# Performance work log

Measured on AMD Instinct MI355X. Metric: run time of the kernel, lower is better.

## Reference

```python
import jax, jax.numpy as jnp
import numpy as np

E = 128  # embed_size


def setup_inputs() -> dict:
    key = jax.random.key(0)
    ks = jax.random.split(key, 20)
    NU, NI, NEV = 100000, 50000, 4096
    s = 0.05  # weight scale so softplus(dot) stays well-conditioned
    inp = {
        "user_emb": jax.random.normal(ks[0], (NU, E), jnp.float32) * s,
        "item_emb": jax.random.normal(ks[1], (NI, E), jnp.float32) * s,
        "ugru_wi": jax.random.normal(ks[2], (3 * E, E), jnp.float32) * s,
        "ugru_wh": jax.random.normal(ks[3], (3 * E, E), jnp.float32) * s,
        "ugru_bi": jax.random.normal(ks[4], (3 * E,), jnp.float32) * s,
        "ugru_bh": jax.random.normal(ks[5], (3 * E,), jnp.float32) * s,
        "igru_wi": jax.random.normal(ks[6], (3 * E, E), jnp.float32) * s,
        "igru_wh": jax.random.normal(ks[7], (3 * E, E), jnp.float32) * s,
        "igru_bi": jax.random.normal(ks[8], (3 * E,), jnp.float32) * s,
        "igru_bh": jax.random.normal(ks[9], (3 * E,), jnp.float32) * s,
        "t1_w": jax.random.normal(ks[10], (E, 2 * E), jnp.float32) * s,
        "t1_b": jax.random.normal(ks[11], (E,), jnp.float32) * s,
        "t2_w": jax.random.normal(ks[12], (32, E), jnp.float32) * s,
        "t2_b": jax.random.normal(ks[13], (32,), jnp.float32) * s,
        "t3_w": jax.random.normal(ks[14], (1, 32), jnp.float32) * s,
        "t3_b": jax.random.normal(ks[15], (1,), jnp.float32) * s,
        "user_ids": jax.random.randint(ks[16], (NEV,), 0, NU, jnp.int32),
        "item_ids": jax.random.randint(ks[17], (NEV,), 0, NI, jnp.int32),
    }
    return inp


def _gru(x, h, wi, wh, bi, bh):
    # torch.nn.GRUCell math, single sample: x,h [E]; wi,wh [3E,E]
    gi = wi @ x + bi
    gh = wh @ h + bh
    ir, iz, inn = jnp.split(gi, 3)
    hr, hz, hn = jnp.split(gh, 3)
    r = jax.nn.sigmoid(ir + hr)
    z = jax.nn.sigmoid(iz + hz)
    n = jnp.tanh(inn + r * hn)
    return (1.0 - z) * n + z * h


def reference(user_emb, item_emb, ugru_wi, ugru_wh, ugru_bi, ugru_bh,
              igru_wi, igru_wh, igru_bi, igru_bh,
              t1_w, t1_b, t2_w, t2_b, t3_w, t3_b,
              user_ids, item_ids):
    # Sequential event processing: per-event gather of user/item embedding,
    # Rayleigh base compatibility score, MLP (transForm1/2/3) branch score,
    # coupled GRUCell updates scattered back into the embedding tables.
    def step(carry, ev):
        U, V = carry
        u_id, i_id = ev
        u = U[u_id]          # [E] gather (dict-cache lookup in original)
        v = V[i_id]          # [E]
        comp = jax.nn.softplus(jnp.dot(u, v)) + 1e-10  # base_compatibility
        loss = -jnp.log(comp)                           # -log p(event)
        cat = jnp.concatenate([u, v])                   # [2E]
        h = jax.nn.relu(t1_w @ cat + t1_b)              # transForm1 + act
        h = jax.nn.relu(t2_w @ h + t2_b)                # transForm2 + act
        score = jax.nn.sigmoid(t3_w @ h + t3_b)[0]      # transForm3
        nu = _gru(v, u, ugru_wi, ugru_wh, ugru_bi, ugru_bh)  # user_cell
        nv = _gru(u, v, igru_wi, igru_wh, igru_bi, igru_bh)  # item_cell
        U = U.at[u_id].set(nu)  # coevolution scatter
        V = V.at[i_id].set(nv)
        return (U, V), jnp.stack([loss, score])

    (_, _), outs = jax.lax.scan(step, (user_emb, item_emb),
                                (user_ids, item_ids))
    return outs  # [num_events, 2] : (-log comp, branch score)
```

## Files before the change

kernel.cpp:

```cpp
#include <hip/hip_runtime.h>
#include <math.h>

#define EMB 128
#define MAXEV 4096
#define GEV 16

struct Hdr { int nl0; int nl1; int ncomp2; };

typedef __attribute__((ext_vector_type(8))) short bf16x8;
typedef __attribute__((ext_vector_type(4))) float f32x4;

__device__ __forceinline__ float sigmoidf_(float x) { return 1.0f / (1.0f + expf(-x)); }
__device__ __forceinline__ float softplusf_(float x) {
    return (x > 0.f) ? x + log1pf(expf(-x)) : log1pf(expf(x));
}
__device__ __forceinline__ unsigned short f2bf(float f) {
    unsigned int u = __float_as_uint(f);
    u += 0x7FFFu + ((u >> 16) & 1u);
    return (unsigned short)(u >> 16);
}
__device__ __forceinline__ float bf2f(unsigned short s) {
    return __uint_as_float((unsigned int)s << 16);
}

__global__ __launch_bounds__(64) void prev_kernel(
    const int* __restrict__ uids, const int* __restrict__ iids,
    int* __restrict__ prevu, int* __restrict__ previ, int nev,
    const float* __restrict__ Wuh, const float* __restrict__ Wii,
    const float* __restrict__ Wui, const float* __restrict__ Wih,
    const float* __restrict__ T1w, const float* __restrict__ T2w,
    unsigned short* __restrict__ wb_uh, unsigned short* __restrict__ wb_ii,
    unsigned short* __restrict__ wb_ui, unsigned short* __restrict__ wb_ih,
    unsigned short* __restrict__ t1wb, unsigned short* __restrict__ t2wb)
{
    int t = blockIdx.x;
    int lane = threadIdx.x;

    {
        int gid = t * 64 + lane;
        if (gid < 58368) {
            const float* src; unsigned short* dst; int q;
            if (gid < 49152) {
                int m = gid / 12288; q = gid - m * 12288;
                src = (m == 0) ? Wuh : (m == 1) ? Wii : (m == 2) ? Wui : Wih;
                dst = (m == 0) ? wb_uh : (m == 1) ? wb_ii : (m == 2) ? wb_ui : wb_ih;
            } else if (gid < 57344) { q = gid - 49152; src = T1w; dst = t1wb; }
            else                    { q = gid - 57344; src = T2w; dst = t2wb; }
            float4 v = ((const float4*)src)[q];
            *(ushort4*)(dst + (size_t)q * 4) =
                make_ushort4(f2bf(v.x), f2bf(v.y), f2bf(v.z), f2bf(v.w));
        }
    }

    if (t >= nev) return;
    int myu = uids[t], myi = iids[t];
    int bu = -1, bi = -1;
    for (int j = lane; j < t; j += 64) {
        if (uids[j] == myu) bu = j;
        if (iids[j] == myi) bi = j;
    }
    for (int off = 32; off; off >>= 1) {
        bu = max(bu, __shfl_xor(bu, off));
        bi = max(bi, __shfl_xor(bi, off));
    }
    if (lane == 0) { prevu[t] = bu; previ[t] = bi; }
}

__global__ __launch_bounds__(1024) void setup_kernel(
    const int* __restrict__ prevu, const int* __restrict__ previ,
    int* __restrict__ order0, int* __restrict__ order1,
    int* __restrict__ tail2Order, int* __restrict__ compStart,
    Hdr* __restrict__ hdr, int nev)
{
    __shared__ int   lab[MAXEV];
    __shared__ int   tmpT[MAXEV];
    __shared__ int   t2l[MAXEV];
    __shared__ short slev[MAXEV];
    __shared__ int   schanged, sn0, sn1, sn2, sntl;

    int tid = threadIdx.x;
    for (int t = tid; t < nev; t += 1024) slev[t] = 0;
    if (tid == 0) { sn0 = 0; sn1 = 0; sn2 = 0; sntl = 0; }
    __syncthreads();

    for (int t = tid; t < nev; t += 1024) {
        if (prevu[t] >= 0 || previ[t] >= 0) tmpT[atomicAdd(&sntl, 1)] = t;
        else                                 order0[atomicAdd(&sn0, 1)] = t;
    }
    __syncthreads();
    int ntl = sntl;

    for (int it = 0; it < nev; ++it) {
        if (tid == 0) schanged = 0;
        __syncthreads();
        for (int i = tid; i < ntl; i += 1024) {
            int t = tmpT[i];
            int pu = prevu[t], pi = previ[t];
            int nl = 0;
            if (pu >= 0) nl = slev[pu] + 1;
            if (pi >= 0) { int c = slev[pi] + 1; nl = nl > c ? nl : c; }
            if (nl > (int)slev[t]) { slev[t] = (short)nl; schanged = 1; }
        }
        __syncthreads();
        if (!schanged) break;
        __syncthreads();
    }

    for (int i = tid; i < ntl; i += 1024) {
        int t = tmpT[i];
        if (slev[t] == 1)      order1[atomicAdd(&sn1, 1)] = t;
        else if (slev[t] >= 2) t2l[atomicAdd(&sn2, 1)] = t;
    }
    __syncthreads();
    int n2 = sn2;

    for (int i = tid; i < n2; i += 1024) lab[t2l[i]] = t2l[i];
    __syncthreads();
    for (int it = 0; it < nev; ++it) {
        if (tid == 0) schanged = 0;
        __syncthreads();
        for (int i = tid; i < n2; i += 1024) {
            int t = t2l[i];
            int m = lab[t];
            int pu = prevu[t], pi = previ[t];
            bool eu = (pu >= 0 && slev[pu] >= 2);
            bool ei = (pi >= 0 && slev[pi] >= 2);
            if (eu) m = min(m, lab[pu]);
            if (ei) m = min(m, lab[pi]);
            if (m < lab[t]) { atomicMin(&lab[t], m); schanged = 1; }
            if (eu && m < lab[pu]) { atomicMin(&lab[pu], m); schanged = 1; }
            if (ei && m < lab[pi]) { atomicMin(&lab[pi], m); schanged = 1; }
        }
        __syncthreads();
        if (!schanged) break;
        __syncthreads();
    }

    for (int i = tid; i < n2; i += 1024) tmpT[i] = (lab[t2l[i]] << 12) | t2l[i];
    __syncthreads();
    for (int i = tid; i < n2; i += 1024) {
        int k = tmpT[i], r = 0;
        for (int j = 0; j < n2; ++j) r += (tmpT[j] < k);
        tail2Order[r] = k & 0xFFF;
    }
    __syncthreads();

    if (tid == 0) {
        int nc = 0;
        for (int i = 0; i < n2; ++i)
            if (i == 0 || lab[tail2Order[i]] != lab[tail2Order[i - 1]])
                compStart[nc++] = i;
        compStart[nc] = n2;
        hdr->ncomp2 = nc;
        hdr->nl0 = sn0;
        hdr->nl1 = sn1;
    }
}

__global__ __launch_bounds__(256) void gru_fused_kernel(
    const float* __restrict__ U0, const float* __restrict__ V0,
    const unsigned short* __restrict__ wb_ui, const unsigned short* __restrict__ wb_uh,
    const unsigned short* __restrict__ wb_ii, const unsigned short* __restrict__ wb_ih,
    const float* __restrict__ bui, const float* __restrict__ buh,
    const float* __restrict__ bii, const float* __restrict__ bih,
    const unsigned short* __restrict__ t1wb, const float* __restrict__ T1b,
    const unsigned short* __restrict__ t2wb, const float* __restrict__ T2b,
    const float* __restrict__ T3w, const float* __restrict__ T3b,
    const int* __restrict__ uids, const int* __restrict__ iids,
    const int* __restrict__ prevu, const int* __restrict__ previ,
    const float* NUr, const float* NVr,
    const int* __restrict__ order, const int* __restrict__ cnt_p,
    float* NU, float* NV, float* __restrict__ out)
{
    __shared__ __align__(16) unsigned short xbu[GEV][136];
    __shared__ __align__(16) unsigned short xbv[GEV][136];
    __shared__ __align__(16) float gg[GEV][772];
    unsigned short (*h1b)[136] = (unsigned short (*)[136])&gg[0][0];
    float (*h2s)[36] = (float (*)[36])&gg[2][0];

    int cnt = *cnt_p;
    int e0 = blockIdx.x * GEV;
    if (e0 >= cnt) return;

    int tid = threadIdx.x;
    int ev = tid >> 4, c8 = (tid & 15) * 8;

    {
        int e = e0 + ev;
        int t = -1;
        float4 a0, a1, c0, c1;
        if (e < cnt) {
            t = order[e];
            int pu = prevu[t], pi = previ[t];
            const float* up = (pu < 0 ? U0 + (size_t)uids[t] * EMB : NUr + (size_t)pu * EMB) + c8;
            const float* vp = (pi < 0 ? V0 + (size_t)iids[t] * EMB : NVr + (size_t)pi * EMB) + c8;
            a0 = ((const float4*)up)[0]; a1 = ((const float4*)up)[1];
            c0 = ((const float4*)vp)[0]; c1 = ((const float4*)vp)[1];
        } else {
            a0 = make_float4(0.f, 0.f, 0.f, 0.f); a1 = a0; c0 = a0; c1 = a0;
        }
        *(ushort4*)&xbu[ev][c8]     = make_ushort4(f2bf(a0.x), f2bf(a0.y), f2bf(a0.z), f2bf(a0.w));
        *(ushort4*)&xbu[ev][c8 + 4] = make_ushort4(f2bf(a1.x), f2bf(a1.y), f2bf(a1.z), f2bf(a1.w));
        *(ushort4*)&xbv[ev][c8]     = make_ushort4(f2bf(c0.x), f2bf(c0.y), f2bf(c0.z), f2bf(c0.w));
        *(ushort4*)&xbv[ev][c8 + 4] = make_ushort4(f2bf(c1.x), f2bf(c1.y), f2bf(c1.z), f2bf(c1.w));
        float dp = a0.x * c0.x + a0.y * c0.y + a0.z * c0.z + a0.w * c0.w
                 + a1.x * c1.x + a1.y * c1.y + a1.z * c1.z + a1.w * c1.w;
        dp += __shfl_xor(dp, 1); dp += __shfl_xor(dp, 2);
        dp += __shfl_xor(dp, 4); dp += __shfl_xor(dp, 8);
        if ((tid & 15) == 0 && t >= 0)
            out[2 * (size_t)t] = -logf(softplusf_(dp) + 1e-10f);
    }
    __syncthreads();

    int w = tid >> 6, l = tid & 63;
    int lr = l & 15, lk = (l >> 4) * 8;

    for (int ph = 0; ph < 2; ++ph) {
        const unsigned short* Wi = ph ? wb_ii : wb_ui;
        const unsigned short* Wh = ph ? wb_ih : wb_uh;
        const unsigned short (*Xi)[136] = ph ? xbu : xbv;
        const unsigned short (*Xh)[136] = ph ? xbv : xbu;

        f32x4 acc[12] = {};
        #pragma unroll
        for (int kk = 0; kk < 4; ++kk) {
            bf16x8 ai = *(const bf16x8*)&Xi[lr][kk * 32 + lk];
            bf16x8 ah = *(const bf16x8*)&Xh[lr][kk * 32 + lk];
            #pragma unroll
            for (int j = 0; j < 12; ++j) {
                int nt = w * 12 + j;
                bool ish = nt >= 24;
                int brow = (ish ? nt - 24 : nt) * 16 + lr;
                const unsigned short* W = ish ? Wh : Wi;
                bf16x8 b = *(const bf16x8*)(W + (size_t)brow * EMB + kk * 32 + lk);
                acc[j] = __builtin_amdgcn_mfma_f32_16x16x32_bf16(ish ? ah : ai, b, acc[j], 0, 0, 0);
            }
        }
        #pragma unroll
        for (int j = 0; j < 12; ++j) {
            int nt = w * 12 + j;
            #pragma unroll
            for (int i = 0; i < 4; ++i)
                gg[(l >> 4) * 4 + i][nt * 16 + lr] = acc[j][i];
        }
        __syncthreads();

        {
            int e = e0 + ev;
            if (e < cnt) {
                int t = order[e];
                const float* bi = ph ? bii : bui;
                const float* bh = ph ? bih : buh;
                float* N = ph ? NV : NU;
                const unsigned short (*xh)[136] = ph ? xbv : xbu;
                #pragma unroll
                for (int i = 0; i < 8; ++i) {
                    int ch = c8 + i;
                    float r_ = sigmoidf_(gg[ev][ch] + bi[ch] + gg[ev][384 + ch] + bh[ch]);
                    float z_ = sigmoidf_(gg[ev][128 + ch] + bi[128 + ch] + gg[ev][512 + ch] + bh[128 + ch]);
                    float n_ = tanhf(gg[ev][256 + ch] + bi[256 + ch] + r_ * (gg[ev][640 + ch] + bh[256 + ch]));
                    float h = bf2f(xh[ev][ch]);
                    N[(size_t)t * EMB + ch] = (1.f - z_) * n_ + z_ * h;
                }
            }
        }
        __syncthreads();
    }

    {
        f32x4 acc1[2] = {};
        #pragma unroll
        for (int kh = 0; kh < 8; ++kh) {
            bf16x8 a = (kh < 4) ? *(const bf16x8*)&xbu[lr][kh * 32 + lk]
                                : *(const bf16x8*)&xbv[lr][(kh - 4) * 32 + lk];
            #pragma unroll
            for (int n = 0; n < 2; ++n) {
                int nt = w * 2 + n;
                bf16x8 b = *(const bf16x8*)(t1wb + (size_t)(nt * 16 + lr) * 256 + kh * 32 + lk);
                acc1[n] = __builtin_amdgcn_mfma_f32_16x16x32_bf16(a, b, acc1[n], 0, 0, 0);
            }
        }
        #pragma unroll
        for (int n = 0; n < 2; ++n) {
            int col = (w * 2 + n) * 16 + lr;
            float bb = T1b[col];
            #pragma unroll
            for (int i = 0; i < 4; ++i)
                h1b[(l >> 4) * 4 + i][col] = f2bf(fmaxf(acc1[n][i] + bb, 0.f));
        }
    }
    __syncthreads();

    if (w < 2) {
        f32x4 acc2 = {};
        #pragma unroll
        for (int kk = 0; kk < 4; ++kk) {
            bf16x8 a = *(const bf16x8*)&h1b[lr][kk * 32 + lk];
            bf16x8 b = *(const bf16x8*)(t2wb + (size_t)(w * 16 + lr) * 128 + kk * 32 + lk);
            acc2 = __builtin_amdgcn_mfma_f32_16x16x32_bf16(a, b, acc2, 0, 0, 0);
        }
        int col = w * 16 + lr;
        float bb = T2b[col];
        #pragma unroll
        for (int i = 0; i < 4; ++i)
            h2s[(l >> 4) * 4 + i][col] = fmaxf(acc2[i] + bb, 0.f);
    }
    __syncthreads();

    if (tid < 64) {
        int evl = tid >> 2, q4 = tid & 3;
        float p = 0.f;
        #pragma unroll
        for (int i = 0; i < 8; ++i) {
            int ch = q4 * 8 + i;
            p = fmaf(T3w[ch], h2s[evl][ch], p);
        }
        p += __shfl_xor(p, 1); p += __shfl_xor(p, 2);
        int e = e0 + evl;
        if (q4 == 0 && e < cnt)
            out[2 * (size_t)order[e] + 1] = sigmoidf_(p + T3b[0]);
    }
}

__global__ __launch_bounds__(1024) void tail2_kernel(
    const float* __restrict__ U0,  const float* __restrict__ V0,
    const unsigned short* __restrict__ wb_ui, const unsigned short* __restrict__ wb_uh,
    const float* __restrict__ bui, const float* __restrict__ buh,
    const unsigned short* __restrict__ wb_ii, const unsigned short* __restrict__ wb_ih,
    const float* __restrict__ bii, const float* __restrict__ bih,
    const unsigned short* __restrict__ t1wb, const float* __restrict__ T1b,
    const float* __restrict__ T2w, const float* __restrict__ T2b,
    const float* __restrict__ T3w, const float* __restrict__ T3b,
    const int* __restrict__ uids,  const int* __restrict__ iids,
    const int* __restrict__ prevu, const int* __restrict__ previ,
    const int* __restrict__ tail2Order, const int* __restrict__ compStart,
    const Hdr* __restrict__ hdr,
    float* __restrict__ NU, float* __restrict__ NV, float* __restrict__ out)
{
    __shared__ __align__(16) float su[EMB];
    __shared__ __align__(16) float sv[EMB];
    __shared__ float gg[1536];
    int tid = threadIdx.x;
    int ncomp = hdr->ncomp2;

    int g = tid >> 4, j = tid & 15;
    int mat = g >> 4;
    const unsigned short* W = (mat == 0) ? wb_ui : (mat == 1) ? wb_uh
                            : (mat == 2) ? wb_ii : wb_ih;

    for (int c = blockIdx.x; c < ncomp; c += gridDim.x) {
        int kb = compStart[c], ke = compStart[c + 1];
        for (int k = kb; k < ke; ++k) {
            int t = tail2Order[k];
            int pu = prevu[t], pi = previ[t];
            const float* up = (pu < 0) ? U0 + (size_t)uids[t] * EMB : NU + (size_t)pu * EMB;
            const float* vp = (pi < 0) ? V0 + (size_t)iids[t] * EMB : NV + (size_t)pi * EMB;
            __syncthreads();
            if (tid < EMB)        su[tid] = up[tid];
            else if (tid < 2*EMB) sv[tid - EMB] = vp[tid - EMB];
            __syncthreads();

            const float* x = (mat == 1 || mat == 2) ? su : sv;
            float x8[8];
            #pragma unroll
            for (int i = 0; i < 8; ++i) x8[i] = x[j * 8 + i];

            #pragma unroll 1
            for (int b = 0; b < 2; ++b) {
                int rbase = (g & 15) * 24 + b * 12;
                bf16x8 wv[12];
                #pragma unroll
                for (int q = 0; q < 12; ++q)
                    wv[q] = *(const bf16x8*)(W + (size_t)(rbase + q) * EMB + j * 8);
                #pragma unroll
                for (int q = 0; q < 12; ++q) {
                    float s = bf2f((unsigned short)wv[q][0]) * x8[0]
                            + bf2f((unsigned short)wv[q][1]) * x8[1]
                            + bf2f((unsigned short)wv[q][2]) * x8[2]
                            + bf2f((unsigned short)wv[q][3]) * x8[3]
                            + bf2f((unsigned short)wv[q][4]) * x8[4]
                            + bf2f((unsigned short)wv[q][5]) * x8[5]
                            + bf2f((unsigned short)wv[q][6]) * x8[6]
                            + bf2f((unsigned short)wv[q][7]) * x8[7];
                    s += __shfl_xor(s, 1); s += __shfl_xor(s, 2);
                    s += __shfl_xor(s, 4); s += __shfl_xor(s, 8);
                    if (j == (q & 15)) gg[mat * 384 + rbase + q] = s;
                }
            }
            __syncthreads();

            if (tid < EMB) {
                int e = tid;
                float r_ = sigmoidf_(gg[e] + bui[e] + gg[384 + e] + buh[e]);
                float z_ = sigmoidf_(gg[128 + e] + bui[128 + e] + gg[512 + e] + buh[128 + e]);
                float n_ = tanhf(gg[256 + e] + bui[256 + e] + r_ * (gg[640 + e] + buh[256 + e]));
                NU[(size_t)t * EMB + e] = (1.f - z_) * n_ + z_ * su[e];
            } else if (tid < 2*EMB) {
                int e = tid - EMB;
                float r_ = sigmoidf_(gg[768 + e] + bii[e] + gg[1152 + e] + bih[e]);
                float z_ = sigmoidf_(gg[896 + e] + bii[128 + e] + gg[1280 + e] + bih[128 + e]);
                float n_ = tanhf(gg[1024 + e] + bii[256 + e] + r_ * (gg[1408 + e] + bih[256 + e]));
                NV[(size_t)t * EMB + e] = (1.f - z_) * n_ + z_ * sv[e];
            }
            __syncthreads();

            if (tid < 64) {
                float p = su[tid] * sv[tid] + su[tid + 64] * sv[tid + 64];
                p += __shfl_xor(p, 1);  p += __shfl_xor(p, 2);
                p += __shfl_xor(p, 4);  p += __shfl_xor(p, 8);
                p += __shfl_xor(p, 16); p += __shfl_xor(p, 32);
                if (tid == 0) out[2 * (size_t)t] = -logf(softplusf_(p) + 1e-10f);
            }
            {
                int r = tid >> 3, kq = tid & 7;
                const float* xx = (kq < 4) ? su : sv;
                int off = (kq < 4) ? 0 : 128;
                float s = 0.f;
                #pragma unroll
                for (int m = 0; m < 4; ++m) {
                    bf16x8 wv = *(const bf16x8*)(t1wb + (size_t)r * 256 + kq * 32 + m * 8);
                    #pragma unroll
                    for (int i = 0; i < 8; ++i)
                        s = fmaf(bf2f((unsigned short)wv[i]),
                                 xx[kq * 32 + m * 8 + i - off], s);
                }
                s += __shfl_xor(s, 1); s += __shfl_xor(s, 2); s += __shfl_xor(s, 4);
                if (kq == 0) gg[r] = fmaxf(s + T1b[r], 0.f);
            }
            __syncthreads();
            {
                int r2 = tid >> 5, kq = tid & 31;
                float4 wv = *(const float4*)(T2w + (size_t)r2 * 128 + kq * 4);
                float s = wv.x * gg[kq * 4]     + wv.y * gg[kq * 4 + 1]
                        + wv.z * gg[kq * 4 + 2] + wv.w * gg[kq * 4 + 3];
                s += __shfl_xor(s, 1); s += __shfl_xor(s, 2);
                s += __shfl_xor(s, 4); s += __shfl_xor(s, 8); s += __shfl_xor(s, 16);
                if (kq == 0) gg[200 + r2] = fmaxf(s + T2b[r2], 0.f);
            }
            __syncthreads();
            if (tid < 32) {
                float p = T3w[tid] * gg[200 + tid];
                p += __shfl_xor(p, 1); p += __shfl_xor(p, 2);
                p += __shfl_xor(p, 4); p += __shfl_xor(p, 8); p += __shfl_xor(p, 16);
                if (tid == 0) out[2 * (size_t)t + 1] = sigmoidf_(p + T3b[0]);
            }
        }
    }
}

extern "C" void kernel_launch(void* const* d_in, const int* in_sizes, int n_in,
                              void* d_out, int out_size, void* d_ws, size_t ws_size,
                              hipStream_t stream)
{
    const float* U0  = (const float*)d_in[0];
    const float* V0  = (const float*)d_in[1];
    const float* Wui = (const float*)d_in[2];
    const float* Wuh = (const float*)d_in[3];
    const float* bui = (const float*)d_in[4];
    const float* buh = (const float*)d_in[5];
    const float* Wii = (const float*)d_in[6];
    const float* Wih = (const float*)d_in[7];
    const float* bii = (const float*)d_in[8];
    const float* bih = (const float*)d_in[9];
    const float* T1w = (const float*)d_in[10];
    const float* T1b = (const float*)d_in[11];
    const float* T2w = (const float*)d_in[12];
    const float* T2b = (const float*)d_in[13];
    const float* T3w = (const float*)d_in[14];
    const float* T3b = (const float*)d_in[15];
    const int* uids  = (const int*)d_in[16];
    const int* iids  = (const int*)d_in[17];
    int nev = in_sizes[16];

    char* ws = (char*)d_ws;
    int* base = (int*)ws;
    int* prevu      = base;
    int* previ      = base + MAXEV;
    int* order0     = base + 2 * MAXEV;
    int* order1     = base + 3 * MAXEV;
    int* tail2Order = base + 4 * MAXEV;
    int* compStart  = base + 5 * MAXEV;
    Hdr* hdr        = (Hdr*)(base + 6 * MAXEV + 4);
    float* NU = (float*)(ws + (160 << 10));
    float* NV = NU + (size_t)MAXEV * EMB;
    unsigned short* wb_uh = (unsigned short*)(NV + (size_t)MAXEV * EMB);
    unsigned short* wb_ii = wb_uh + 384 * EMB;
    unsigned short* wb_ui = wb_ii + 384 * EMB;
    unsigned short* wb_ih = wb_ui + 384 * EMB;
    unsigned short* t1wb  = wb_ih + 384 * EMB;
    unsigned short* t2wb  = t1wb + EMB * 256;
    float* out = (float*)d_out;

    prev_kernel<<<MAXEV, 64, 0, stream>>>(
        uids, iids, prevu, previ, nev,
        Wuh, Wii, Wui, Wih, T1w, T2w,
        wb_uh, wb_ii, wb_ui, wb_ih, t1wb, t2wb);
    setup_kernel<<<1, 1024, 0, stream>>>(prevu, previ, order0, order1,
                                         tail2Order, compStart, hdr, nev);

    gru_fused_kernel<<<MAXEV / GEV, 256, 0, stream>>>(
        U0, V0, wb_ui, wb_uh, wb_ii, wb_ih, bui, buh, bii, bih,
        t1wb, T1b, t2wb, T2b, T3w, T3b,
        uids, iids, prevu, previ, NU, NV, order0, &hdr->nl0, NU, NV, out);

    gru_fused_kernel<<<MAXEV / GEV, 256, 0, stream>>>(
        U0, V0, wb_ui, wb_uh, wb_ii, wb_ih, bui, buh, bii, bih,
        t1wb, T1b, t2wb, T2b, T3w, T3b,
        uids, iids, prevu, previ, NU, NV, order1, &hdr->nl1, NU, NV, out);

    tail2_kernel<<<64, 1024, 0, stream>>>(
        U0, V0, wb_ui, wb_uh, bui, buh, wb_ii, wb_ih, bii, bih,
        t1wb, T1b, T2w, T2b, T3w, T3b,
        uids, iids, prevu, previ, tail2Order, compStart, hdr, NU, NV, out);
}
```

Baseline: 101.7 us.

## Move MLP and loss out of serial tail GRU loop into batched per-wave pass

The tail kernel now runs only the GRU updates in its serial per-component loop. Afterward it computes the base loss and the three-layer MLP score for 16 events at a time, one wavefront per event, by regathering the pre-update embeddings into shared memory. This shortens the serial dependency chain and removes several block-wide barriers from each step. The second MLP layer now uses bf16 weights instead of fp32, which adds small rounding differences.

```diff
diff --git a/kernel.cpp b/kernel.cpp
--- a/kernel.cpp
+++ b/kernel.cpp
@@ -329,7 +329,7 @@
     const unsigned short* __restrict__ wb_ii, const unsigned short* __restrict__ wb_ih,
     const float* __restrict__ bii, const float* __restrict__ bih,
     const unsigned short* __restrict__ t1wb, const float* __restrict__ T1b,
-    const float* __restrict__ T2w, const float* __restrict__ T2b,
+    const unsigned short* __restrict__ t2wb, const float* __restrict__ T2b,
     const float* __restrict__ T3w, const float* __restrict__ T3b,
     const int* __restrict__ uids,  const int* __restrict__ iids,
     const int* __restrict__ prevu, const int* __restrict__ previ,
@@ -340,6 +340,8 @@
     __shared__ __align__(16) float su[EMB];
     __shared__ __align__(16) float sv[EMB];
     __shared__ float gg[1536];
+    __shared__ __align__(16) float sxe[16][256];
+    __shared__ float sh1[16][EMB];
     int tid = threadIdx.x;
     int ncomp = hdr->ncomp2;
 
@@ -350,6 +352,7 @@
 
     for (int c = blockIdx.x; c < ncomp; c += gridDim.x) {
         int kb = compStart[c], ke = compStart[c + 1];
+
         for (int k = kb; k < ke; ++k) {
             int t = tail2Order[k];
             int pu = prevu[t], pi = previ[t];
@@ -402,47 +405,67 @@
                 float n_ = tanhf(gg[1024 + e] + bii[256 + e] + r_ * (gg[1408 + e] + bih[256 + e]));
                 NV[(size_t)t * EMB + e] = (1.f - z_) * n_ + z_ * sv[e];
             }
-            __syncthreads();
-
-            if (tid < 64) {
-                float p = su[tid] * sv[tid] + su[tid + 64] * sv[tid + 64];
-                p += __shfl_xor(p, 1);  p += __shfl_xor(p, 2);
-                p += __shfl_xor(p, 4);  p += __shfl_xor(p, 8);
-                p += __shfl_xor(p, 16); p += __shfl_xor(p, 32);
-                if (tid == 0) out[2 * (size_t)t] = -logf(softplusf_(p) + 1e-10f);
-            }
-            {
-                int r = tid >> 3, kq = tid & 7;
-                const float* xx = (kq < 4) ? su : sv;
-                int off = (kq < 4) ? 0 : 128;
-                float s = 0.f;
-                #pragma unroll
-                for (int m = 0; m < 4; ++m) {
-                    bf16x8 wv = *(const bf16x8*)(t1wb + (size_t)r * 256 + kq * 32 + m * 8);
-                    #pragma unroll
-                    for (int i = 0; i < 8; ++i)
-                        s = fmaf(bf2f((unsigned short)wv[i]),
-                                 xx[kq * 32 + m * 8 + i - off], s);
-                }
-                s += __shfl_xor(s, 1); s += __shfl_xor(s, 2); s += __shfl_xor(s, 4);
-                if (kq == 0) gg[r] = fmaxf(s + T1b[r], 0.f);
-            }
+        }
+
+        for (int kk0 = kb; kk0 < ke; kk0 += 16) {
             __syncthreads();
             {
-                int r2 = tid >> 5, kq = tid & 31;
-                float4 wv = *(const float4*)(T2w + (size_t)r2 * 128 + kq * 4);
-                float s = wv.x * gg[kq * 4]     + wv.y * gg[kq * 4 + 1]
-                        + wv.z * gg[kq * 4 + 2] + wv.w * gg[kq * 4 + 3];
-                s += __shfl_xor(s, 1); s += __shfl_xor(s, 2);
-                s += __shfl_xor(s, 4); s += __shfl_xor(s, 8); s += __shfl_xor(s, 16);
-                if (kq == 0) gg[200 + r2] = fmaxf(s + T2b[r2], 0.f);
+                int ev = tid >> 6, c4 = (tid & 63) * 4;
+                int k = kk0 + ev;
+                if (k < ke) {
+                    int t = tail2Order[k];
+                    int pu = prevu[t], pi = previ[t];
+                    const float* up = (pu < 0) ? U0 + (size_t)uids[t] * EMB : NU + (size_t)pu * EMB;
+                    const float* vp = (pi < 0) ? V0 + (size_t)iids[t] * EMB : NV + (size_t)pi * EMB;
+                    const float* src = (c4 < EMB) ? up + c4 : vp + (c4 - EMB);
+                    *(float4*)&sxe[ev][c4] = *(const float4*)src;
+                }
             }
             __syncthreads();
-            if (tid < 32) {
-                float p = T3w[tid] * gg[200 + tid];
-                p += __shfl_xor(p, 1); p += __shfl_xor(p, 2);
-                p += __shfl_xor(p, 4); p += __shfl_xor(p, 8); p += __shfl_xor(p, 16);
-                if (tid == 0) out[2 * (size_t)t + 1] = sigmoidf_(p + T3b[0]);
+
+            int wv2 = tid >> 6, l = tid & 63;
+            int k = kk0 + wv2;
+            if (k < ke) {
+                int t = tail2Order[k];
+                const float* sx = sxe[wv2];
+                {
+                    float p = sx[l] * sx[128 + l] + sx[l + 64] * sx[192 + l];
+                    p += __shfl_xor(p, 1);  p += __shfl_xor(p, 2);
+                    p += __shfl_xor(p, 4);  p += __shfl_xor(p, 8);
+                    p += __shfl_xor(p, 16); p += __shfl_xor(p, 32);
+                    if (l == 0) out[2 * (size_t)t] = -logf(softplusf_(p) + 1e-10f);
+                }
+                {
+                    float s0 = 0.f, s1 = 0.f;
+                    #pragma unroll 4
+                    for (int m = 0; m < 32; ++m) {
+                        bf16x8 w0 = *(const bf16x8*)(t1wb + (size_t)l * 256 + m * 8);
+                        bf16x8 w1 = *(const bf16x8*)(t1wb + (size_t)(l + 64) * 256 + m * 8);
+                        #pragma unroll
+                        for (int i = 0; i < 8; ++i) {
+                            float xv = sx[m * 8 + i];
+                            s0 = fmaf(bf2f((unsigned short)w0[i]), xv, s0);
+                            s1 = fmaf(bf2f((unsigned short)w1[i]), xv, s1);
+                        }
+                    }
+                    sh1[wv2][l]      = fmaxf(s0 + T1b[l], 0.f);
+                    sh1[wv2][l + 64] = fmaxf(s1 + T1b[l + 64], 0.f);
+                }
+                if (l < 32) {
+                    float s = 0.f;
+                    #pragma unroll 4
+                    for (int m = 0; m < 16; ++m) {
+                        bf16x8 wv = *(const bf16x8*)(t2wb + (size_t)l * 128 + m * 8);
+                        #pragma unroll
+                        for (int i = 0; i < 8; ++i)
+                            s = fmaf(bf2f((unsigned short)wv[i]), sh1[wv2][m * 8 + i], s);
+                    }
+                    float h2 = fmaxf(s + T2b[l], 0.f);
+                    float p = T3w[l] * h2;
+                    p += __shfl_xor(p, 1); p += __shfl_xor(p, 2);
+                    p += __shfl_xor(p, 4); p += __shfl_xor(p, 8); p += __shfl_xor(p, 16);
+                    if (l == 0) out[2 * (size_t)t + 1] = sigmoidf_(p + T3b[0]);
+                }
             }
         }
     }
@@ -510,6 +533,6 @@
 
     tail2_kernel<<<64, 1024, 0, stream>>>(
         U0, V0, wb_ui, wb_uh, bui, buh, wb_ii, wb_ih, bii, bih,
-        t1wb, T1b, T2w, T2b, T3w, T3b,
+        t1wb, T1b, t2wb, T2b, T3w, T3b,
         uids, iids, prevu, previ, tail2Order, compStart, hdr, NU, NV, out);
 }
```

After: 104.2 us. 2.4% more time.

## Drop level-1 batch pass; route all dependent events through component tail kernel

Applied to the files above, without the earlier changes.

The level-based split is removed. Events with no prior occurrence go to the batched GRU kernel, and every dependent event is grouped into connected components that the sequential tail kernel processes. This drops one launch of the fused kernel and the level-propagation loop in setup, and the tail grid grows from 64 to 256 blocks to cover the larger set of components. The trade-off is that level-1 events, which used to be batched, now run one at a time inside their component, and the O(n^2) rank sort now runs over more elements.

```diff
diff --git a/kernel.cpp b/kernel.cpp
--- a/kernel.cpp
+++ b/kernel.cpp
@@ -5,7 +5,7 @@
 #define MAXEV 4096
 #define GEV 16
 
-struct Hdr { int nl0; int nl1; int ncomp2; };
+struct Hdr { int nl0; int ncomp; };
 
 typedef __attribute__((ext_vector_type(8))) short bf16x8;
 typedef __attribute__((ext_vector_type(4))) float f32x4;
@@ -68,63 +68,39 @@
 
 __global__ __launch_bounds__(1024) void setup_kernel(
     const int* __restrict__ prevu, const int* __restrict__ previ,
-    int* __restrict__ order0, int* __restrict__ order1,
-    int* __restrict__ tail2Order, int* __restrict__ compStart,
-    Hdr* __restrict__ hdr, int nev)
+    int* __restrict__ order0, int* __restrict__ tailOrder,
+    int* __restrict__ compStart, Hdr* __restrict__ hdr, int nev)
 {
-    __shared__ int   lab[MAXEV];
-    __shared__ int   tmpT[MAXEV];
-    __shared__ int   t2l[MAXEV];
-    __shared__ short slev[MAXEV];
-    __shared__ int   schanged, sn0, sn1, sn2, sntl;
+    __shared__ int  lab[MAXEV];
+    __shared__ int  tmpT[MAXEV];
+    __shared__ int  t2l[MAXEV];
+    __shared__ char istail[MAXEV];
+    __shared__ int  schanged, sn0, sntl;
 
     int tid = threadIdx.x;
-    for (int t = tid; t < nev; t += 1024) slev[t] = 0;
-    if (tid == 0) { sn0 = 0; sn1 = 0; sn2 = 0; sntl = 0; }
+    if (tid == 0) { sn0 = 0; sntl = 0; }
     __syncthreads();
 
     for (int t = tid; t < nev; t += 1024) {
-        if (prevu[t] >= 0 || previ[t] >= 0) tmpT[atomicAdd(&sntl, 1)] = t;
-        else                                 order0[atomicAdd(&sn0, 1)] = t;
+        bool tl = (prevu[t] >= 0 || previ[t] >= 0);
+        istail[t] = tl;
+        if (tl) t2l[atomicAdd(&sntl, 1)] = t;
+        else    order0[atomicAdd(&sn0, 1)] = t;
     }
     __syncthreads();
     int ntl = sntl;
 
+    for (int i = tid; i < ntl; i += 1024) lab[t2l[i]] = t2l[i];
+    __syncthreads();
     for (int it = 0; it < nev; ++it) {
         if (tid == 0) schanged = 0;
         __syncthreads();
         for (int i = tid; i < ntl; i += 1024) {
-            int t = tmpT[i];
-            int pu = prevu[t], pi = previ[t];
-            int nl = 0;
-            if (pu >= 0) nl = slev[pu] + 1;
-            if (pi >= 0) { int c = slev[pi] + 1; nl = nl > c ? nl : c; }
-            if (nl > (int)slev[t]) { slev[t] = (short)nl; schanged = 1; }
-        }
-        __syncthreads();
-        if (!schanged) break;
-        __syncthreads();
-    }
-
-    for (int i = tid; i < ntl; i += 1024) {
-        int t = tmpT[i];
-        if (slev[t] == 1)      order1[atomicAdd(&sn1, 1)] = t;
-        else if (slev[t] >= 2) t2l[atomicAdd(&sn2, 1)] = t;
-    }
-    __syncthreads();
-    int n2 = sn2;
-
-    for (int i = tid; i < n2; i += 1024) lab[t2l[i]] = t2l[i];
-    __syncthreads();
-    for (int it = 0; it < nev; ++it) {
-        if (tid == 0) schanged = 0;
-        __syncthreads();
-        for (int i = tid; i < n2; i += 1024) {
             int t = t2l[i];
             int m = lab[t];
             int pu = prevu[t], pi = previ[t];
-            bool eu = (pu >= 0 && slev[pu] >= 2);
-            bool ei = (pi >= 0 && slev[pi] >= 2);
+            bool eu = (pu >= 0 && istail[pu]);
+            bool ei = (pi >= 0 && istail[pi]);
             if (eu) m = min(m, lab[pu]);
             if (ei) m = min(m, lab[pi]);
             if (m < lab[t]) { atomicMin(&lab[t], m); schanged = 1; }
@@ -136,24 +112,23 @@
         __syncthreads();
     }
 
-    for (int i = tid; i < n2; i += 1024) tmpT[i] = (lab[t2l[i]] << 12) | t2l[i];
-    __syncthreads();
-    for (int i = tid; i < n2; i += 1024) {
+    for (int i = tid; i < ntl; i += 1024) tmpT[i] = (lab[t2l[i]] << 12) | t2l[i];
+    __syncthreads();
+    for (int i = tid; i < ntl; i += 1024) {
         int k = tmpT[i], r = 0;
-        for (int j = 0; j < n2; ++j) r += (tmpT[j] < k);
-        tail2Order[r] = k & 0xFFF;
+        for (int j = 0; j < ntl; ++j) r += (tmpT[j] < k);
+        tailOrder[r] = k & 0xFFF;
     }
     __syncthreads();
 
     if (tid == 0) {
         int nc = 0;
-        for (int i = 0; i < n2; ++i)
-            if (i == 0 || lab[tail2Order[i]] != lab[tail2Order[i - 1]])
+        for (int i = 0; i < ntl; ++i)
+            if (i == 0 || lab[tailOrder[i]] != lab[tailOrder[i - 1]])
                 compStart[nc++] = i;
-        compStart[nc] = n2;
-        hdr->ncomp2 = nc;
+        compStart[nc] = ntl;
+        hdr->ncomp = nc;
         hdr->nl0 = sn0;
-        hdr->nl1 = sn1;
     }
 }
 
@@ -167,10 +142,8 @@
     const unsigned short* __restrict__ t2wb, const float* __restrict__ T2b,
     const float* __restrict__ T3w, const float* __restrict__ T3b,
     const int* __restrict__ uids, const int* __restrict__ iids,
-    const int* __restrict__ prevu, const int* __restrict__ previ,
-    const float* NUr, const float* NVr,
     const int* __restrict__ order, const int* __restrict__ cnt_p,
-    float* NU, float* NV, float* __restrict__ out)
+    float* __restrict__ NU, float* __restrict__ NV, float* __restrict__ out)
 {
     __shared__ __align__(16) unsigned short xbu[GEV][136];
     __shared__ __align__(16) unsigned short xbv[GEV][136];
@@ -191,9 +164,8 @@
         float4 a0, a1, c0, c1;
         if (e < cnt) {
             t = order[e];
-            int pu = prevu[t], pi = previ[t];
-            const float* up = (pu < 0 ? U0 + (size_t)uids[t] * EMB : NUr + (size_t)pu * EMB) + c8;
-            const float* vp = (pi < 0 ? V0 + (size_t)iids[t] * EMB : NVr + (size_t)pi * EMB) + c8;
+            const float* up = U0 + (size_t)uids[t] * EMB + c8;
+            const float* vp = V0 + (size_t)iids[t] * EMB + c8;
             a0 = ((const float4*)up)[0]; a1 = ((const float4*)up)[1];
             c0 = ((const float4*)vp)[0]; c1 = ((const float4*)vp)[1];
         } else {
@@ -322,7 +294,7 @@
     }
 }
 
-__global__ __launch_bounds__(1024) void tail2_kernel(
+__global__ __launch_bounds__(1024) void tail_kernel(
     const float* __restrict__ U0,  const float* __restrict__ V0,
     const unsigned short* __restrict__ wb_ui, const unsigned short* __restrict__ wb_uh,
     const float* __restrict__ bui, const float* __restrict__ buh,
@@ -333,7 +305,7 @@
     const float* __restrict__ T3w, const float* __restrict__ T3b,
     const int* __restrict__ uids,  const int* __restrict__ iids,
     const int* __restrict__ prevu, const int* __restrict__ previ,
-    const int* __restrict__ tail2Order, const int* __restrict__ compStart,
+    const int* __restrict__ tailOrder, const int* __restrict__ compStart,
     const Hdr* __restrict__ hdr,
     float* __restrict__ NU, float* __restrict__ NV, float* __restrict__ out)
 {
@@ -341,7 +313,7 @@
     __shared__ __align__(16) float sv[EMB];
     __shared__ float gg[1536];
     int tid = threadIdx.x;
-    int ncomp = hdr->ncomp2;
+    int ncomp = hdr->ncomp;
 
     int g = tid >> 4, j = tid & 15;
     int mat = g >> 4;
@@ -351,7 +323,7 @@
     for (int c = blockIdx.x; c < ncomp; c += gridDim.x) {
         int kb = compStart[c], ke = compStart[c + 1];
         for (int k = kb; k < ke; ++k) {
-            int t = tail2Order[k];
+            int t = tailOrder[k];
             int pu = prevu[t], pi = previ[t];
             const float* up = (pu < 0) ? U0 + (size_t)uids[t] * EMB : NU + (size_t)pu * EMB;
             const float* vp = (pi < 0) ? V0 + (size_t)iids[t] * EMB : NV + (size_t)pi * EMB;
@@ -474,13 +446,12 @@
 
     char* ws = (char*)d_ws;
     int* base = (int*)ws;
-    int* prevu      = base;
-    int* previ      = base + MAXEV;
-    int* order0     = base + 2 * MAXEV;
-    int* order1     = base + 3 * MAXEV;
-    int* tail2Order = base + 4 * MAXEV;
-    int* compStart  = base + 5 * MAXEV;
-    Hdr* hdr        = (Hdr*)(base + 6 * MAXEV + 4);
+    int* prevu     = base;
+    int* previ     = base + MAXEV;
+    int* order0    = base + 2 * MAXEV;
+    int* tailOrder = base + 3 * MAXEV;
+    int* compStart = base + 4 * MAXEV;
+    Hdr* hdr       = (Hdr*)(base + 5 * MAXEV + 4);
     float* NU = (float*)(ws + (160 << 10));
     float* NV = NU + (size_t)MAXEV * EMB;
     unsigned short* wb_uh = (unsigned short*)(NV + (size_t)MAXEV * EMB);
@@ -495,21 +466,16 @@
         uids, iids, prevu, previ, nev,
         Wuh, Wii, Wui, Wih, T1w, T2w,
         wb_uh, wb_ii, wb_ui, wb_ih, t1wb, t2wb);
-    setup_kernel<<<1, 1024, 0, stream>>>(prevu, previ, order0, order1,
-                                         tail2Order, compStart, hdr, nev);
+    setup_kernel<<<1, 1024, 0, stream>>>(prevu, previ, order0, tailOrder,
+                                         compStart, hdr, nev);
 
     gru_fused_kernel<<<MAXEV / GEV, 256, 0, stream>>>(
         U0, V0, wb_ui, wb_uh, wb_ii, wb_ih, bui, buh, bii, bih,
         t1wb, T1b, t2wb, T2b, T3w, T3b,
-        uids, iids, prevu, previ, NU, NV, order0, &hdr->nl0, NU, NV, out);
-
-    gru_fused_kernel<<<MAXEV / GEV, 256, 0, stream>>>(
-        U0, V0, wb_ui, wb_uh, wb_ii, wb_ih, bui, buh, bii, bih,
-        t1wb, T1b, t2wb, T2b, T3w, T3b,
-        uids, iids, prevu, previ, NU, NV, order1, &hdr->nl1, NU, NV, out);
-
-    tail2_kernel<<<64, 1024, 0, stream>>>(
+        uids, iids, order0, &hdr->nl0, NU, NV, out);
+
+    tail_kernel<<<256, 1024, 0, stream>>>(
         U0, V0, wb_ui, wb_uh, bui, buh, wb_ii, wb_ih, bii, bih,
         t1wb, T1b, T2w, T2b, T3w, T3b,
-        uids, iids, prevu, previ, tail2Order, compStart, hdr, NU, NV, out);
-}
+        uids, iids, prevu, previ, tailOrder, compStart, hdr, NU, NV, out);
+}
```

Measured after the change: 135.9 us. 1.34x slower.
